# Performance work log

Hardware: AMD Instinct MI355X
Metric: run time of the kernel (lower is better)

Reference implementation:

```python
import jax, jax.numpy as jnp
import numpy as np

D = 32
B = 4096
T = 256
HIDDEN = 64
DT = 0.005


def setup_inputs() -> dict:
    key = jax.random.key(0)
    ks = jax.random.split(key, 6)
    s1 = 1.0 / np.sqrt(D + 1)
    s2 = 1.0 / np.sqrt(HIDDEN)
    return {
        "z0": jax.random.normal(ks[0], (B, D), dtype=jnp.float32),
        "ts": jnp.arange(T, dtype=jnp.float32) * DT,
        "noise": jax.random.normal(ks[1], (T - 1, B, D), dtype=jnp.float32),
        "W1": jax.random.normal(ks[2], (D + 1, HIDDEN), dtype=jnp.float32) * s1,
        "b1": jnp.zeros((HIDDEN,), dtype=jnp.float32),
        "W2": jax.random.normal(ks[3], (HIDDEN, HIDDEN), dtype=jnp.float32) * s2,
        "b2": jnp.zeros((HIDDEN,), dtype=jnp.float32),
        "W3": jax.random.normal(ks[4], (HIDDEN, D), dtype=jnp.float32) * s2,
        "b3": jnp.zeros((D,), dtype=jnp.float32),
        "log_std": jnp.full((D,), -1.0, dtype=jnp.float32),
    }


def reference(z0, ts, noise, W1, b1, W2, b2, W3, b3, log_std):
    """Euler-Maruyama integration of the posterior SDE.

    dz = f_phi(t, z) dt + diag(exp(log_std)) dW,  dW = sqrt(dt) * noise.
    Returns ys of shape [T, B, D] with ys[0] = z0 (matches torchsde.sdeint).
    """
    std = jnp.exp(log_std)  # [D], constant diagonal diffusion
    dts = ts[1:] - ts[:-1]  # [T-1]

    def drift(t, y):
        # MLP on cat([t, y]): Linear -> tanh -> Linear -> tanh -> Linear
        tt = jnp.broadcast_to(t, (y.shape[0], 1)).astype(y.dtype)
        h = jnp.tanh(jnp.concatenate([tt, y], axis=-1) @ W1 + b1)
        h = jnp.tanh(h @ W2 + b2)
        return h @ W3 + b3  # [B, D]

    def step(y, xs):
        t, dt, dw = xs
        y_next = y + drift(t, y) * dt + std * jnp.sqrt(dt) * dw
        return y_next, y_next

    _, ys = jax.lax.scan(step, z0, (ts[:-1], dts, noise))
    return jnp.concatenate([z0[None], ys], axis=0)  # [T, B, D]
```

## Files before the change

kernel.cpp:

```cpp
#include <hip/hip_runtime.h>

#define NB 4096
#define NT 256

typedef __bf16 bf16x8 __attribute__((ext_vector_type(8)));
typedef __bf16 bf16x4 __attribute__((ext_vector_type(4)));
typedef float f32x4 __attribute__((ext_vector_type(4)));
typedef unsigned int u32;
typedef unsigned int u32x4 __attribute__((ext_vector_type(4)));
typedef unsigned long long u64;

static __device__ __forceinline__ f32x4 mfma16(bf16x8 a, bf16x8 b, f32x4 c) {
  return __builtin_amdgcn_mfma_f32_16x16x32_bf16(a, b, c, 0, 0, 0);
}

#define LDS_BARRIER() asm volatile("s_waitcnt lgkmcnt(0)\n\ts_barrier" ::: "memory")

static __device__ __forceinline__ float sigc(float x) {
  float e = __builtin_amdgcn_exp2f(x * 2.885390082f);
  return __builtin_amdgcn_rcpf(e + 1.0f);
}

static __device__ __forceinline__ u64 pack4s(f32x4 v) {
  bf16x4 p;
  p[0] = (__bf16)sigc(v[0]);
  p[1] = (__bf16)sigc(v[1]);
  p[2] = (__bf16)sigc(v[2]);
  p[3] = (__bf16)sigc(v[3]);
  return __builtin_bit_cast(u64, p);
}

static __device__ __forceinline__ bf16x8 frag2(u64 lo, u64 hi) {
  u32x4 v;
  v[0] = (u32)lo; v[1] = (u32)(lo >> 32);
  v[2] = (u32)hi; v[3] = (u32)(hi >> 32);
  return __builtin_bit_cast(bf16x8, v);
}

__global__ __launch_bounds__(256) void sde_kernel(
    const float* __restrict__ z0, const float* __restrict__ ts,
    const float* __restrict__ noise, const float* __restrict__ W1,
    const float* __restrict__ b1, const float* __restrict__ W2,
    const float* __restrict__ b2, const float* __restrict__ W3,
    const float* __restrict__ b3, const float* __restrict__ log_std,
    float* __restrict__ out) {
  (void)ts;
  __shared__ u64 h1x[4][64];
  __shared__ u64 h2x[4][64];

  const int lane = threadIdx.x & 63;
  const int wv = threadIdx.x >> 6;
  const int c = lane & 15;
  const int g = lane >> 4;
  const int R = blockIdx.x * 16 + c;

  bf16x8 a1;
  bf16x8 a2[2];
  bf16x8 a3[2][2];
#pragma unroll
  for (int j = 0; j < 8; ++j) {
    int k = 16 * (j >> 2) + 4 * g + (j & 3);
    a1[j] = (__bf16)W1[(1 + k) * 64 + 16 * wv + c];
  }
#pragma unroll
  for (int kf = 0; kf < 2; ++kf)
#pragma unroll
    for (int j = 0; j < 8; ++j) {
      int k = 32 * kf + 16 * (j >> 2) + 4 * g + (j & 3);
      a2[kf][j] = (__bf16)(-2.0f * W2[k * 64 + 16 * wv + c]);
    }
#pragma unroll
  for (int ot = 0; ot < 2; ++ot)
#pragma unroll
    for (int kf = 0; kf < 2; ++kf)
#pragma unroll
      for (int j = 0; j < 8; ++j) {
        int k = 32 * kf + 16 * (j >> 2) + 4 * g + (j & 3);
        a3[ot][kf][j] = (__bf16)(-2.0f * W3[k * 32 + 16 * ot + c]);
      }

  f32x4 b1v, w1r0;
#pragma unroll
  for (int r = 0; r < 4; ++r) {
    int d = 16 * wv + 4 * g + r;
    b1v[r] = b1[d];
    w1r0[r] = W1[d];
  }
  f32x4 b2s;
#pragma unroll
  for (int r = 0; r < 4; ++r) {
    int d = 16 * wv + 4 * g + r;
    float s = b2[d];
    for (int j = 0; j < 64; ++j) s += W2[j * 64 + d];
    b2s[r] = s;
  }
  f32x4 b3s[2], stdv[2];
#pragma unroll
  for (int ot = 0; ot < 2; ++ot)
#pragma unroll
    for (int r = 0; r < 4; ++r) {
      int d = 16 * ot + 4 * g + r;
      float s = b3[d];
      for (int j = 0; j < 64; ++j) s += W3[j * 32 + d];
      b3s[ot][r] = s;
      stdv[ot][r] = expf(log_std[d]);
    }
  const f32x4 zero4 = {0.0f, 0.0f, 0.0f, 0.0f};

  f32x4 y0v = *reinterpret_cast<const f32x4*>(z0 + (size_t)R * 32 + 4 * g);
  f32x4 y1v = *reinterpret_cast<const f32x4*>(z0 + (size_t)R * 32 + 16 + 4 * g);
  if (wv == 0)
    *reinterpret_cast<f32x4*>(out + (size_t)R * 32 + 4 * g) = y0v;
  if (wv == 1)
    *reinterpret_cast<f32x4*>(out + (size_t)R * 32 + 16 + 4 * g) = y1v;

  bf16x8 yb;
#pragma unroll
  for (int j = 0; j < 8; ++j)
    yb[j] = (__bf16)((j >> 2) ? y1v[j & 3] : y0v[j & 3]);

  f32x4 pend0 = y0v, pend1 = y1v;
  float* pendp = out + (size_t)R * 32 + 4 * g;

  const float* nzp0 = noise + ((size_t)0 * NB + R) * 32 + 4 * g;
  f32x4 nz0 = *reinterpret_cast<const f32x4*>(nzp0);
  f32x4 nz1 = *reinterpret_cast<const f32x4*>(nzp0 + 16);

  for (int t = 0; t < NT - 1; ++t) {
    float tcur = (float)t * 0.005f;

    f32x4 d1 = mfma16(a1, yb, b1v + tcur * w1r0);
    h1x[wv][lane] = pack4s(d1);
    LDS_BARRIER();

    u64 q0 = h1x[0][lane], q1 = h1x[1][lane];
    u64 q2 = h1x[2][lane], q3 = h1x[3][lane];
    if (wv == 0) *reinterpret_cast<f32x4*>(pendp) = pend0;
    if (wv == 1) *reinterpret_cast<f32x4*>(pendp + 16) = pend1;
    int tn = (t < NT - 2) ? (t + 1) : (NT - 2);
    const float* nzp = noise + ((size_t)tn * NB + R) * 32 + 4 * g;
    f32x4 nzn0 = *reinterpret_cast<const f32x4*>(nzp);
    f32x4 nzn1 = *reinterpret_cast<const f32x4*>(nzp + 16);
    float dtv = (float)(t + 1) * 0.005f - tcur;
    float sdt = sqrtf(dtv);
    bf16x8 hb0 = frag2(q0, q1);
    bf16x8 hb1 = frag2(q2, q3);
    f32x4 accA = mfma16(a2[0], hb0, b2s);
    f32x4 accB = mfma16(a2[1], hb1, zero4);
    h2x[wv][lane] = pack4s(accA + accB);
    LDS_BARRIER();

    u64 p0 = h2x[0][lane], p1 = h2x[1][lane];
    u64 p2 = h2x[2][lane], p3 = h2x[3][lane];
    f32x4 s0 = stdv[0] * sdt;
    f32x4 s1 = stdv[1] * sdt;
    bf16x8 gb0 = frag2(p0, p1);
    bf16x8 gb1 = frag2(p2, p3);
    f32x4 dA0 = mfma16(a3[0][0], gb0, b3s[0]);
    f32x4 dB0 = mfma16(a3[0][1], gb1, zero4);
    f32x4 dA1 = mfma16(a3[1][0], gb0, b3s[1]);
    f32x4 dB1 = mfma16(a3[1][1], gb1, zero4);
    f32x4 d30 = dA0 + dB0;
    f32x4 d31 = dA1 + dB1;

    y0v = y0v + d30 * dtv + s0 * nz0;
    y1v = y1v + d31 * dtv + s1 * nz1;
#pragma unroll
    for (int j = 0; j < 8; ++j)
      yb[j] = (__bf16)((j >> 2) ? y1v[j & 3] : y0v[j & 3]);
    pend0 = y0v;
    pend1 = y1v;
    pendp = out + ((size_t)(t + 1) * NB + R) * 32 + 4 * g;
    nz0 = nzn0;
    nz1 = nzn1;
  }
  if (wv == 0) *reinterpret_cast<f32x4*>(pendp) = pend0;
  if (wv == 1) *reinterpret_cast<f32x4*>(pendp + 16) = pend1;
}

extern "C" void kernel_launch(void* const* d_in, const int* in_sizes, int n_in,
                              void* d_out, int out_size, void* d_ws, size_t ws_size,
                              hipStream_t stream) {
  (void)in_sizes; (void)n_in; (void)out_size; (void)d_ws; (void)ws_size;
  const float* z0   = (const float*)d_in[0];
  const float* ts   = (const float*)d_in[1];
  const float* nz   = (const float*)d_in[2];
  const float* W1   = (const float*)d_in[3];
  const float* b1   = (const float*)d_in[4];
  const float* W2   = (const float*)d_in[5];
  const float* b2   = (const float*)d_in[6];
  const float* W3   = (const float*)d_in[7];
  const float* b3   = (const float*)d_in[8];
  const float* lstd = (const float*)d_in[9];
  float* out = (float*)d_out;
  hipLaunchKernelGGL(sde_kernel, dim3(NB / 16), dim3(256), 0, stream,
                     z0, ts, nz, W1, b1, W2, b2, W3, b3, lstd, out);
}
```

Measured before the change: 185.5 us.

## Process four row tiles per block to amortize barriers, fold exp2 scale into weights

Each block now handles four 16-row tiles (TT=4) per timestep, interleaving their MFMAs between the same two LDS barriers. The aim is to amortize barrier and latency costs over more independent work and to expose ILP across tiles. The grid shrinks from 256 to 64 blocks, so on a GPU with many CUs fewer CUs are occupied and per-block register pressure rises. Separately, the tanh exp2 scale constant is folded into the weights and biases, which removes one multiply per activation.

```diff
diff --git a/kernel.cpp b/kernel.cpp
--- a/kernel.cpp
+++ b/kernel.cpp
@@ -2,6 +2,7 @@
 
 #define NB 4096
 #define NT 256
+#define TT 4
 
 typedef __bf16 bf16x8 __attribute__((ext_vector_type(8)));
 typedef __bf16 bf16x4 __attribute__((ext_vector_type(4)));
@@ -10,15 +11,16 @@
 typedef unsigned int u32x4 __attribute__((ext_vector_type(4)));
 typedef unsigned long long u64;
 
+#define SC 2.885390082f
+
 static __device__ __forceinline__ f32x4 mfma16(bf16x8 a, bf16x8 b, f32x4 c) {
   return __builtin_amdgcn_mfma_f32_16x16x32_bf16(a, b, c, 0, 0, 0);
 }
 
 #define LDS_BARRIER() asm volatile("s_waitcnt lgkmcnt(0)\n\ts_barrier" ::: "memory")
 
-static __device__ __forceinline__ float sigc(float x) {
-  float e = __builtin_amdgcn_exp2f(x * 2.885390082f);
-  return __builtin_amdgcn_rcpf(e + 1.0f);
+static __device__ __forceinline__ float sigc(float xs) {
+  return __builtin_amdgcn_rcpf(__builtin_amdgcn_exp2f(xs) + 1.0f);
 }
 
 static __device__ __forceinline__ u64 pack4s(f32x4 v) {
@@ -45,14 +47,14 @@
     const float* __restrict__ b3, const float* __restrict__ log_std,
     float* __restrict__ out) {
   (void)ts;
-  __shared__ u64 h1x[4][64];
-  __shared__ u64 h2x[4][64];
+  __shared__ u64 h1x[TT][4][64];
+  __shared__ u64 h2x[TT][4][64];
 
   const int lane = threadIdx.x & 63;
   const int wv = threadIdx.x >> 6;
   const int c = lane & 15;
   const int g = lane >> 4;
-  const int R = blockIdx.x * 16 + c;
+  const int Rb = blockIdx.x * (16 * TT) + c;
 
   bf16x8 a1;
   bf16x8 a2[2];
@@ -60,14 +62,14 @@
 #pragma unroll
   for (int j = 0; j < 8; ++j) {
     int k = 16 * (j >> 2) + 4 * g + (j & 3);
-    a1[j] = (__bf16)W1[(1 + k) * 64 + 16 * wv + c];
+    a1[j] = (__bf16)(SC * W1[(1 + k) * 64 + 16 * wv + c]);
   }
 #pragma unroll
   for (int kf = 0; kf < 2; ++kf)
 #pragma unroll
     for (int j = 0; j < 8; ++j) {
       int k = 32 * kf + 16 * (j >> 2) + 4 * g + (j & 3);
-      a2[kf][j] = (__bf16)(-2.0f * W2[k * 64 + 16 * wv + c]);
+      a2[kf][j] = (__bf16)(-2.0f * SC * W2[k * 64 + 16 * wv + c]);
     }
 #pragma unroll
   for (int ot = 0; ot < 2; ++ot)
@@ -83,8 +85,8 @@
 #pragma unroll
   for (int r = 0; r < 4; ++r) {
     int d = 16 * wv + 4 * g + r;
-    b1v[r] = b1[d];
-    w1r0[r] = W1[d];
+    b1v[r] = SC * b1[d];
+    w1r0[r] = SC * W1[d];
   }
   f32x4 b2s;
 #pragma unroll
@@ -92,7 +94,7 @@
     int d = 16 * wv + 4 * g + r;
     float s = b2[d];
     for (int j = 0; j < 64; ++j) s += W2[j * 64 + d];
-    b2s[r] = s;
+    b2s[r] = SC * s;
   }
   f32x4 b3s[2], stdv[2];
 #pragma unroll
@@ -107,75 +109,94 @@
     }
   const f32x4 zero4 = {0.0f, 0.0f, 0.0f, 0.0f};
 
-  f32x4 y0v = *reinterpret_cast<const f32x4*>(z0 + (size_t)R * 32 + 4 * g);
-  f32x4 y1v = *reinterpret_cast<const f32x4*>(z0 + (size_t)R * 32 + 16 + 4 * g);
-  if (wv == 0)
-    *reinterpret_cast<f32x4*>(out + (size_t)R * 32 + 4 * g) = y0v;
-  if (wv == 1)
-    *reinterpret_cast<f32x4*>(out + (size_t)R * 32 + 16 + 4 * g) = y1v;
-
-  bf16x8 yb;
-#pragma unroll
-  for (int j = 0; j < 8; ++j)
-    yb[j] = (__bf16)((j >> 2) ? y1v[j & 3] : y0v[j & 3]);
-
-  f32x4 pend0 = y0v, pend1 = y1v;
-  float* pendp = out + (size_t)R * 32 + 4 * g;
-
-  const float* nzp0 = noise + ((size_t)0 * NB + R) * 32 + 4 * g;
-  f32x4 nz0 = *reinterpret_cast<const f32x4*>(nzp0);
-  f32x4 nz1 = *reinterpret_cast<const f32x4*>(nzp0 + 16);
+  f32x4 y0v[TT], y1v[TT], nz0[TT], nz1[TT];
+  bf16x8 yb[TT];
+#pragma unroll
+  for (int tl = 0; tl < TT; ++tl) {
+    const int R = Rb + 16 * tl;
+    y0v[tl] = *reinterpret_cast<const f32x4*>(z0 + (size_t)R * 32 + 4 * g);
+    y1v[tl] = *reinterpret_cast<const f32x4*>(z0 + (size_t)R * 32 + 16 + 4 * g);
+#pragma unroll
+    for (int j = 0; j < 8; ++j)
+      yb[tl][j] = (__bf16)((j >> 2) ? y1v[tl][j & 3] : y0v[tl][j & 3]);
+    const float* nzp = noise + ((size_t)0 * NB + R) * 32 + 4 * g;
+    nz0[tl] = *reinterpret_cast<const f32x4*>(nzp);
+    nz1[tl] = *reinterpret_cast<const f32x4*>(nzp + 16);
+  }
 
   for (int t = 0; t < NT - 1; ++t) {
     float tcur = (float)t * 0.005f;
-
-    f32x4 d1 = mfma16(a1, yb, b1v + tcur * w1r0);
-    h1x[wv][lane] = pack4s(d1);
+    f32x4 cinit = b1v + tcur * w1r0;
+
+#pragma unroll
+    for (int tl = 0; tl < TT; ++tl) {
+      f32x4 d1 = mfma16(a1, yb[tl], cinit);
+      h1x[tl][wv][lane] = pack4s(d1);
+    }
     LDS_BARRIER();
 
-    u64 q0 = h1x[0][lane], q1 = h1x[1][lane];
-    u64 q2 = h1x[2][lane], q3 = h1x[3][lane];
-    if (wv == 0) *reinterpret_cast<f32x4*>(pendp) = pend0;
-    if (wv == 1) *reinterpret_cast<f32x4*>(pendp + 16) = pend1;
+    u64 q[TT][4];
+#pragma unroll
+    for (int tl = 0; tl < TT; ++tl)
+#pragma unroll
+      for (int w = 0; w < 4; ++w) q[tl][w] = h1x[tl][w][lane];
+#pragma unroll
+    for (int tl = 0; tl < TT; ++tl) {
+      float* op = out + ((size_t)t * NB + Rb + 16 * tl) * 32 + 4 * g;
+      if (wv == 0) *reinterpret_cast<f32x4*>(op) = y0v[tl];
+      if (wv == 1) *reinterpret_cast<f32x4*>(op + 16) = y1v[tl];
+    }
     int tn = (t < NT - 2) ? (t + 1) : (NT - 2);
-    const float* nzp = noise + ((size_t)tn * NB + R) * 32 + 4 * g;
-    f32x4 nzn0 = *reinterpret_cast<const f32x4*>(nzp);
-    f32x4 nzn1 = *reinterpret_cast<const f32x4*>(nzp + 16);
+    f32x4 nzn0[TT], nzn1[TT];
+#pragma unroll
+    for (int tl = 0; tl < TT; ++tl) {
+      const float* nzp = noise + ((size_t)tn * NB + Rb + 16 * tl) * 32 + 4 * g;
+      nzn0[tl] = *reinterpret_cast<const f32x4*>(nzp);
+      nzn1[tl] = *reinterpret_cast<const f32x4*>(nzp + 16);
+    }
     float dtv = (float)(t + 1) * 0.005f - tcur;
     float sdt = sqrtf(dtv);
-    bf16x8 hb0 = frag2(q0, q1);
-    bf16x8 hb1 = frag2(q2, q3);
-    f32x4 accA = mfma16(a2[0], hb0, b2s);
-    f32x4 accB = mfma16(a2[1], hb1, zero4);
-    h2x[wv][lane] = pack4s(accA + accB);
-    LDS_BARRIER();
-
-    u64 p0 = h2x[0][lane], p1 = h2x[1][lane];
-    u64 p2 = h2x[2][lane], p3 = h2x[3][lane];
     f32x4 s0 = stdv[0] * sdt;
     f32x4 s1 = stdv[1] * sdt;
-    bf16x8 gb0 = frag2(p0, p1);
-    bf16x8 gb1 = frag2(p2, p3);
-    f32x4 dA0 = mfma16(a3[0][0], gb0, b3s[0]);
-    f32x4 dB0 = mfma16(a3[0][1], gb1, zero4);
-    f32x4 dA1 = mfma16(a3[1][0], gb0, b3s[1]);
-    f32x4 dB1 = mfma16(a3[1][1], gb1, zero4);
-    f32x4 d30 = dA0 + dB0;
-    f32x4 d31 = dA1 + dB1;
-
-    y0v = y0v + d30 * dtv + s0 * nz0;
-    y1v = y1v + d31 * dtv + s1 * nz1;
-#pragma unroll
-    for (int j = 0; j < 8; ++j)
-      yb[j] = (__bf16)((j >> 2) ? y1v[j & 3] : y0v[j & 3]);
-    pend0 = y0v;
-    pend1 = y1v;
-    pendp = out + ((size_t)(t + 1) * NB + R) * 32 + 4 * g;
-    nz0 = nzn0;
-    nz1 = nzn1;
-  }
-  if (wv == 0) *reinterpret_cast<f32x4*>(pendp) = pend0;
-  if (wv == 1) *reinterpret_cast<f32x4*>(pendp + 16) = pend1;
+#pragma unroll
+    for (int tl = 0; tl < TT; ++tl) {
+      bf16x8 hb0 = frag2(q[tl][0], q[tl][1]);
+      bf16x8 hb1 = frag2(q[tl][2], q[tl][3]);
+      f32x4 accA = mfma16(a2[0], hb0, b2s);
+      f32x4 accB = mfma16(a2[1], hb1, zero4);
+      h2x[tl][wv][lane] = pack4s(accA + accB);
+    }
+    LDS_BARRIER();
+
+    u64 p[TT][4];
+#pragma unroll
+    for (int tl = 0; tl < TT; ++tl)
+#pragma unroll
+      for (int w = 0; w < 4; ++w) p[tl][w] = h2x[tl][w][lane];
+#pragma unroll
+    for (int tl = 0; tl < TT; ++tl) {
+      bf16x8 gb0 = frag2(p[tl][0], p[tl][1]);
+      bf16x8 gb1 = frag2(p[tl][2], p[tl][3]);
+      f32x4 dA0 = mfma16(a3[0][0], gb0, b3s[0]);
+      f32x4 dB0 = mfma16(a3[0][1], gb1, zero4);
+      f32x4 dA1 = mfma16(a3[1][0], gb0, b3s[1]);
+      f32x4 dB1 = mfma16(a3[1][1], gb1, zero4);
+      y0v[tl] = y0v[tl] + (dA0 + dB0) * dtv + s0 * nz0[tl];
+      y1v[tl] = y1v[tl] + (dA1 + dB1) * dtv + s1 * nz1[tl];
+#pragma unroll
+      for (int j = 0; j < 8; ++j)
+        yb[tl][j] = (__bf16)((j >> 2) ? y1v[tl][j & 3] : y0v[tl][j & 3]);
+      nz0[tl] = nzn0[tl];
+      nz1[tl] = nzn1[tl];
+    }
+  }
+
+#pragma unroll
+  for (int tl = 0; tl < TT; ++tl) {
+    float* op = out + ((size_t)(NT - 1) * NB + Rb + 16 * tl) * 32 + 4 * g;
+    if (wv == 0) *reinterpret_cast<f32x4*>(op) = y0v[tl];
+    if (wv == 1) *reinterpret_cast<f32x4*>(op + 16) = y1v[tl];
+  }
 }
 
 extern "C" void kernel_launch(void* const* d_in, const int* in_sizes, int n_in,
@@ -193,6 +214,6 @@
   const float* b3   = (const float*)d_in[8];
   const float* lstd = (const float*)d_in[9];
   float* out = (float*)d_out;
-  hipLaunchKernelGGL(sde_kernel, dim3(NB / 16), dim3(256), 0, stream,
+  hipLaunchKernelGGL(sde_kernel, dim3(NB / (16 * TT)), dim3(256), 0, stream,
                      z0, ts, nz, W1, b1, W2, b2, W3, b3, lstd, out);
 }
```

Measured after the change: 443.9 us. +139.3%, slower.
